# Performance work log

Measured on AMD Instinct MI355X. Metric: run time of the kernel, lower is better.

The kernel has to match this reference:

```python
import jax, jax.numpy as jnp
import numpy as np
from jax import lax

ALPHA = 0.99  # get_norm_alpha(8000, 80, 1.0): exp(-0.01)=0.99005 -> rounds to 0.99 (<1)
B, C, T, F = 64, 2, 4000, 96


def setup_inputs() -> dict:
    key = jax.random.key(0)
    k1, = jax.random.split(key, 1)
    feat_spec = jax.random.normal(k1, (B, C, T, F), dtype=jnp.float32)
    # make_spec_norm_state(): linspace(unit_norm_init_start, unit_norm_init_end, df_bins)
    state = jnp.linspace(0.001, 0.0001, F, dtype=jnp.float32)[None, None, :]  # [1,1,F]
    return {"feat_spec": feat_spec, "state": state}


def reference(feat_spec, state):
    b, c, t, f = feat_spec.shape
    state0 = jnp.broadcast_to(state, (b, 1, f)).astype(feat_spec.dtype)

    def step(s, x):  # x: [b, c, f], s: [b, 1, f]
        abs2 = jnp.sum(x * x, axis=1, keepdims=True)          # [b, 1, f]
        new_s = abs2 * (1.0 - ALPHA) + s * ALPHA              # EMA of |X|^2
        y = x / jnp.sqrt(new_s)                               # RMS-style norm
        return new_s, y

    xs = jnp.moveaxis(feat_spec, 2, 0)                        # [t, b, c, f]
    final_state, ys = lax.scan(step, state0, xs)
    out = jnp.moveaxis(ys, 0, 2)                              # [b, c, t, f]
    return out, final_state
```

## Files before the change

kernel.cpp:

```cpp
#include <hip/hip_runtime.h>


namespace {
constexpr int Bdim = 64, Cdim = 2, Tdim = 4000, Fdim = 96;
constexpr int K = 200, L = 20;
constexpr int FG = Fdim / 4;
constexpr int CHAINS = Bdim * FG;
constexpr float kAlpha = 0.99f;
constexpr float kOneMinusAlpha = 0.01f;
constexpr float kAlphaL = 0.81790694f;

typedef float v4f __attribute__((ext_vector_type(4)));

__device__ __forceinline__ v4f ld4(const float* p) {
  return *reinterpret_cast<const v4f*>(p);
}
__device__ __forceinline__ v4f ld4_nt(const float* p) {
  return __builtin_nontemporal_load(reinterpret_cast<const v4f*>(p));
}
}

__global__ __launch_bounds__(256) void spec_ema_phase1(
    const float* __restrict__ x, float* __restrict__ bws) {
  const int g = blockIdx.x * 256 + threadIdx.x;
  const int chain = g % CHAINS;
  const int k = g / CHAINS;
  const int b = chain / FG, fg = chain % FG;

  const size_t base =
      ((size_t)b * Cdim * Tdim + (size_t)k * L) * Fdim + (size_t)fg * 4;
  const float* p0 = x + base;
  const float* p1 = p0 + (size_t)Tdim * Fdim;

  v4f s = 0.0f;
#pragma unroll 10
  for (int j = 0; j < L; ++j) {
    v4f x0 = ld4(p0 + (size_t)j * Fdim);
    v4f x1 = ld4(p1 + (size_t)j * Fdim);
    v4f abs2 = x0 * x0 + x1 * x1;
    s = s * kAlpha + abs2 * kOneMinusAlpha;
  }
  *reinterpret_cast<v4f*>(bws + (size_t)g * 4) = s;
}

__global__ __launch_bounds__(256) void spec_ema_phase3(
    const float* __restrict__ x, const float* __restrict__ state,
    const float* __restrict__ bws, float* __restrict__ out) {
  const int g = blockIdx.x * 256 + threadIdx.x;
  const int chain = g % CHAINS;
  const int k = g / CHAINS;
  const int b = chain / FG, fg = chain % FG;

  v4f s = ld4(state + (size_t)fg * 4);
#pragma unroll 4
  for (int m = 0; m < k; ++m) {
    v4f bm = ld4(bws + ((size_t)m * CHAINS + chain) * 4);
    s = s * kAlphaL + bm;
  }

  const size_t base =
      ((size_t)b * Cdim * Tdim + (size_t)k * L) * Fdim + (size_t)fg * 4;
  const float* p0 = x + base;
  const float* p1 = p0 + (size_t)Tdim * Fdim;
  float* q0 = out + base;
  float* q1 = q0 + (size_t)Tdim * Fdim;

#pragma unroll 5
  for (int j = 0; j < L; ++j) {
    v4f x0 = ld4_nt(p0 + (size_t)j * Fdim);
    v4f x1 = ld4_nt(p1 + (size_t)j * Fdim);
    v4f abs2 = x0 * x0 + x1 * x1;
    s = s * kAlpha + abs2 * kOneMinusAlpha;
    v4f r;
    r.x = rsqrtf(s.x);
    r.y = rsqrtf(s.y);
    r.z = rsqrtf(s.z);
    r.w = rsqrtf(s.w);
    v4f y0 = x0 * r;
    v4f y1 = x1 * r;
    __builtin_nontemporal_store(y0, reinterpret_cast<v4f*>(q0 + (size_t)j * Fdim));
    __builtin_nontemporal_store(y1, reinterpret_cast<v4f*>(q1 + (size_t)j * Fdim));
  }

  if (k == K - 1) {
    *reinterpret_cast<v4f*>(out + (size_t)Bdim * Cdim * Tdim * Fdim +
                            (size_t)b * Fdim + (size_t)fg * 4) = s;
  }
}

extern "C" void kernel_launch(void* const* d_in, const int* in_sizes, int n_in,
                              void* d_out, int out_size, void* d_ws, size_t ws_size,
                              hipStream_t stream) {
  const float* x = (const float*)d_in[0];
  const float* state = (const float*)d_in[1];
  float* out = (float*)d_out;
  float* bws = (float*)d_ws;

  spec_ema_phase1<<<CHAINS * (K - 1) / 256, 256, 0, stream>>>(x, bws);
  spec_ema_phase3<<<CHAINS * K / 256, 256, 0, stream>>>(x, state, bws, out);
}
```

Measured before the change: 368.5 us.

## Fuse two-phase EMA scan into single kernel with decoupled lookback flags

Replaces the separate block-summary and apply kernels with one fused kernel. Each block takes a dynamic virtual block id from an atomic counter, computes its chunk summary, publishes it with agent-scope stores and a release flag, then spin-waits on the flags of its predecessor chunks before combining their summaries and writing normalized output. The input is then read once while it is likely still in cache, rather than read again in a second kernel. In exchange it adds a flag-zeroing launch, spin-wait latency, and serialization through the dependency chain, and it drops the nontemporal loads.

```diff
diff --git a/kernel.cpp b/kernel.cpp
--- a/kernel.cpp
+++ b/kernel.cpp
@@ -6,69 +6,97 @@
 constexpr int K = 200, L = 20;
 constexpr int FG = Fdim / 4;
 constexpr int CHAINS = Bdim * FG;
+constexpr int CB = CHAINS / 256;
+constexpr int NBLK = CB * K;
 constexpr float kAlpha = 0.99f;
 constexpr float kOneMinusAlpha = 0.01f;
 constexpr float kAlphaL = 0.81790694f;
 
 typedef float v4f __attribute__((ext_vector_type(4)));
+typedef unsigned long long u64;
 
 __device__ __forceinline__ v4f ld4(const float* p) {
   return *reinterpret_cast<const v4f*>(p);
 }
-__device__ __forceinline__ v4f ld4_nt(const float* p) {
-  return __builtin_nontemporal_load(reinterpret_cast<const v4f*>(p));
+
+union V4u {
+  v4f v;
+  u64 q[2];
+};
+
+__device__ __forceinline__ void agent_store_v4(float* p, v4f val) {
+  V4u u;
+  u.v = val;
+  u64* q = reinterpret_cast<u64*>(p);
+  __hip_atomic_store(&q[0], u.q[0], __ATOMIC_RELAXED, __HIP_MEMORY_SCOPE_AGENT);
+  __hip_atomic_store(&q[1], u.q[1], __ATOMIC_RELAXED, __HIP_MEMORY_SCOPE_AGENT);
+}
+__device__ __forceinline__ v4f agent_load_v4(const float* p) {
+  const u64* q = reinterpret_cast<const u64*>(p);
+  V4u u;
+  u.q[0] = __hip_atomic_load(&q[0], __ATOMIC_RELAXED, __HIP_MEMORY_SCOPE_AGENT);
+  u.q[1] = __hip_atomic_load(&q[1], __ATOMIC_RELAXED, __HIP_MEMORY_SCOPE_AGENT);
+  return u.v;
 }
 }
 
-__global__ __launch_bounds__(256) void spec_ema_phase1(
-    const float* __restrict__ x, float* __restrict__ bws) {
-  const int g = blockIdx.x * 256 + threadIdx.x;
-  const int chain = g % CHAINS;
-  const int k = g / CHAINS;
+__global__ __launch_bounds__(256) void spec_ema_zero(unsigned int* flags) {
+  const int i = blockIdx.x * 256 + threadIdx.x;
+  if (i < NBLK + 1) flags[i] = 0u;
+}
+
+__global__ __launch_bounds__(256) void spec_ema_fused(
+    const float* __restrict__ x, const float* __restrict__ state,
+    float* __restrict__ bws, unsigned int* __restrict__ flags,
+    float* __restrict__ out) {
+  __shared__ unsigned int s_vb;
+  if (threadIdx.x == 0) s_vb = atomicAdd(&flags[0], 1u);
+  __syncthreads();
+  const int vb = (int)s_vb;
+  const int k = vb / CB, cb = vb % CB;
+  const int chain = cb * 256 + (int)threadIdx.x;
   const int b = chain / FG, fg = chain % FG;
+  unsigned int* fl = flags + 1;
 
   const size_t base =
       ((size_t)b * Cdim * Tdim + (size_t)k * L) * Fdim + (size_t)fg * 4;
   const float* p0 = x + base;
   const float* p1 = p0 + (size_t)Tdim * Fdim;
 
-  v4f s = 0.0f;
+  v4f sB = 0.0f;
 #pragma unroll 10
   for (int j = 0; j < L; ++j) {
     v4f x0 = ld4(p0 + (size_t)j * Fdim);
     v4f x1 = ld4(p1 + (size_t)j * Fdim);
-    v4f abs2 = x0 * x0 + x1 * x1;
-    s = s * kAlpha + abs2 * kOneMinusAlpha;
+    sB = sB * kAlpha + (x0 * x0 + x1 * x1) * kOneMinusAlpha;
   }
-  *reinterpret_cast<v4f*>(bws + (size_t)g * 4) = s;
-}
-
-__global__ __launch_bounds__(256) void spec_ema_phase3(
-    const float* __restrict__ x, const float* __restrict__ state,
-    const float* __restrict__ bws, float* __restrict__ out) {
-  const int g = blockIdx.x * 256 + threadIdx.x;
-  const int chain = g % CHAINS;
-  const int k = g / CHAINS;
-  const int b = chain / FG, fg = chain % FG;
+  agent_store_v4(bws + ((size_t)k * CHAINS + chain) * 4, sB);
+  __syncthreads();
+  if (threadIdx.x == 0)
+    __hip_atomic_store(&fl[vb], 1u, __ATOMIC_RELEASE, __HIP_MEMORY_SCOPE_AGENT);
 
   v4f s = ld4(state + (size_t)fg * 4);
+  if (k > 0) {
+    if ((int)threadIdx.x < k) {
+      while (__hip_atomic_load(&fl[(int)threadIdx.x * CB + cb],
+                               __ATOMIC_RELAXED,
+                               __HIP_MEMORY_SCOPE_AGENT) == 0u)
+        __builtin_amdgcn_s_sleep(4);
+    }
+    __syncthreads();
 #pragma unroll 4
-  for (int m = 0; m < k; ++m) {
-    v4f bm = ld4(bws + ((size_t)m * CHAINS + chain) * 4);
-    s = s * kAlphaL + bm;
+    for (int m = 0; m < k; ++m) {
+      v4f bm = agent_load_v4(bws + ((size_t)m * CHAINS + chain) * 4);
+      s = s * kAlphaL + bm;
+    }
   }
 
-  const size_t base =
-      ((size_t)b * Cdim * Tdim + (size_t)k * L) * Fdim + (size_t)fg * 4;
-  const float* p0 = x + base;
-  const float* p1 = p0 + (size_t)Tdim * Fdim;
   float* q0 = out + base;
   float* q1 = q0 + (size_t)Tdim * Fdim;
-
 #pragma unroll 5
   for (int j = 0; j < L; ++j) {
-    v4f x0 = ld4_nt(p0 + (size_t)j * Fdim);
-    v4f x1 = ld4_nt(p1 + (size_t)j * Fdim);
+    v4f x0 = ld4(p0 + (size_t)j * Fdim);
+    v4f x1 = ld4(p1 + (size_t)j * Fdim);
     v4f abs2 = x0 * x0 + x1 * x1;
     s = s * kAlpha + abs2 * kOneMinusAlpha;
     v4f r;
@@ -76,10 +104,10 @@
     r.y = rsqrtf(s.y);
     r.z = rsqrtf(s.z);
     r.w = rsqrtf(s.w);
-    v4f y0 = x0 * r;
-    v4f y1 = x1 * r;
-    __builtin_nontemporal_store(y0, reinterpret_cast<v4f*>(q0 + (size_t)j * Fdim));
-    __builtin_nontemporal_store(y1, reinterpret_cast<v4f*>(q1 + (size_t)j * Fdim));
+    __builtin_nontemporal_store(x0 * r,
+        reinterpret_cast<v4f*>(q0 + (size_t)j * Fdim));
+    __builtin_nontemporal_store(x1 * r,
+        reinterpret_cast<v4f*>(q1 + (size_t)j * Fdim));
   }
 
   if (k == K - 1) {
@@ -95,7 +123,9 @@
   const float* state = (const float*)d_in[1];
   float* out = (float*)d_out;
   float* bws = (float*)d_ws;
+  unsigned int* flags =
+      (unsigned int*)((char*)d_ws + (size_t)CHAINS * K * 16);
 
-  spec_ema_phase1<<<CHAINS * (K - 1) / 256, 256, 0, stream>>>(x, bws);
-  spec_ema_phase3<<<CHAINS * K / 256, 256, 0, stream>>>(x, state, bws, out);
+  spec_ema_zero<<<(NBLK + 1 + 255) / 256, 256, 0, stream>>>(flags);
+  spec_ema_fused<<<NBLK, 256, 0, stream>>>(x, state, bws, flags, out);
 }
```

New measurement: 474.1 us. +28.7%, slower.
